# Kernel tuning notes

Hardware: AMD Instinct MI355X
Metric: run time of the kernel (lower is better)

## Reference

```python
import jax, jax.numpy as jnp
import numpy as np

LEAKY = 0.1  # leaky_hmm_coefficient (pychain default)


def _fb_objf(x_exp, tfrom, tto, tpdf, tprob, init_p, final_p):
    """Leaky-HMM forward recursion for one sequence.
    x_exp: [T, P] exp'd nnet outputs; transitions are edge lists of length E.
    Returns scalar log-prob of the sequence under the graph.
    """
    S = init_p.shape[0]

    def step(carry, obs):
        alpha, logz = carry  # alpha: [S] normalized occupation probs
        # per-edge contribution: alpha[src] * trans_prob * obs[pdf]
        contrib = alpha[tfrom] * tprob * obs[tpdf]          # [E]
        new_alpha = jnp.zeros(S, alpha.dtype).at[tto].add(contrib)
        tot = new_alpha.sum()
        # leaky-HMM: redistribute a fraction of total mass via initial probs
        new_alpha = new_alpha + LEAKY * tot * init_p
        scale = new_alpha.sum()
        return (new_alpha / scale, logz + jnp.log(scale)), None

    (alpha_T, logz), _ = jax.lax.scan(step, (init_p, jnp.zeros((), x_exp.dtype)), x_exp)
    return logz + jnp.log(jnp.sum(alpha_T * final_p))


def setup_inputs() -> dict:
    key = jax.random.key(0)
    ks = jax.random.split(key, 12)
    B, T, P = 32, 500, 3000
    S_den, E_den = 2000, 40000
    S_num, E_num = 100, 400

    x = jax.random.normal(ks[0], (B, T, P), jnp.float32)

    # denominator graph (shared across batch); every state gets incoming arcs
    den_to = (jnp.arange(E_den, dtype=jnp.int32) % S_den)
    den_from = jax.random.randint(ks[1], (E_den,), 0, S_den, jnp.int32)
    den_pdf = jax.random.randint(ks[2], (E_den,), 0, P, jnp.int32)
    den_prob = jax.random.uniform(ks[3], (E_den,), jnp.float32, 0.1, 1.0)
    den_init = jax.random.uniform(ks[4], (S_den,), jnp.float32, 0.1, 1.0)
    den_init = den_init / den_init.sum()
    den_final = jax.random.uniform(ks[5], (S_den,), jnp.float32, 0.1, 1.0)

    # numerator graphs (one per utterance), batched edge lists
    num_to = jnp.tile(jnp.arange(E_num, dtype=jnp.int32) % S_num, (B, 1))
    num_from = jax.random.randint(ks[6], (B, E_num), 0, S_num, jnp.int32)
    num_pdf = jax.random.randint(ks[7], (B, E_num), 0, P, jnp.int32)
    num_prob = jax.random.uniform(ks[8], (B, E_num), jnp.float32, 0.1, 1.0)
    num_init = jax.random.uniform(ks[9], (B, S_num), jnp.float32, 0.1, 1.0)
    num_init = num_init / num_init.sum(axis=1, keepdims=True)
    num_final = jax.random.uniform(ks[10], (B, S_num), jnp.float32, 0.1, 1.0)

    return {
        "x": x,
        "den_from": den_from, "den_to": den_to, "den_pdf": den_pdf,
        "den_prob": den_prob, "den_init": den_init, "den_final": den_final,
        "num_from": num_from, "num_to": num_to, "num_pdf": num_pdf,
        "num_prob": num_prob, "num_init": num_init, "num_final": num_final,
    }


def reference(x, den_from, den_to, den_pdf, den_prob, den_init, den_final,
              num_from, num_to, num_pdf, num_prob, num_init, num_final):
    B, T, _ = x.shape
    exp_x = jnp.exp(jnp.clip(x, -30.0, 30.0))  # [B, T, P]

    # denominator: shared graph across batch
    den_objf = jax.vmap(_fb_objf, in_axes=(0, None, None, None, None, None, None))(
        exp_x, den_from, den_to, den_pdf, den_prob, den_init, den_final).sum()
    # numerator: per-utterance graph
    num_objf = jax.vmap(_fb_objf, in_axes=(0, 0, 0, 0, 0, 0, 0))(
        exp_x, num_from, num_to, num_pdf, num_prob, num_init, num_final).sum()

    objf = -(num_objf - den_objf)
    return objf / (B * T)  # avg=True
```

## Files before the change

### kernel.cpp

```cpp
#include <hip/hip_runtime.h>


#define LEAKY 0.1f
#define AGENT __HIP_MEMORY_SCOPE_AGENT

constexpr int B = 32, T = 500, P = 3000;
constexpr int S_DEN = 2000;
constexpr int S_NUM = 100, E_NUM = 400;
constexpr int NTH = 1024;
constexpr int NWAVE = NTH / 64;
constexpr int G_DEN = 5;
constexpr int SB = S_DEN / G_DEN;
constexpr int KE = 20;
constexpr int EPT = KE / 2;
constexpr int OBS_T0 = 800;
constexpr int OBS_N = NTH - OBS_T0;
constexpr int OBS_IT = (P + OBS_N - 1) / OBS_N;
constexpr int KE_NUM = 4;
constexpr int NDEN_BLK = B * G_DEN;


__device__ __forceinline__ float clampexp(float x) {
  return __expf(fminf(fmaxf(x, -30.f), 30.f));
}
__device__ __forceinline__ void st_f32(float* p, float v) {
  __hip_atomic_store(p, v, __ATOMIC_RELAXED, AGENT);
}
__device__ __forceinline__ unsigned long long ld_u64(const float* p) {
  return __hip_atomic_load((const unsigned long long*)p, __ATOMIC_RELAXED,
                           AGENT);
}

__device__ __forceinline__ float reduce_1024(float v, float* wpart) {
#pragma unroll
  for (int off = 32; off; off >>= 1) v += __shfl_xor(v, off, 64);
  if ((threadIdx.x & 63) == 0) wpart[threadIdx.x >> 6] = v;
  __syncthreads();
  float s = 0.f;
#pragma unroll
  for (int w = 0; w < NWAVE; ++w) s += wpart[w];
  return s;
}

__device__ void run_den(const float* __restrict__ xb,
                        const int* __restrict__ ef_g,
                        const int* __restrict__ ep_g,
                        const float* __restrict__ epr_g,
                        const float* __restrict__ einit,
                        const float* __restrict__ efinal, int b, int g,
                        float* __restrict__ outs, float* __restrict__ parts_b,
                        float* obsA, float* obsB, float* cur, float* ini_s,
                        float* tmp, float* wpart) {
  const int tid = threadIdx.x;
  const bool gat = tid < 2 * SB;
  const bool own = tid < SB;
  const bool cons = tid < S_DEN / 2;
  const int jloc = own ? tid : (gat ? tid - SB : 0);
  const int khalf = (tid >= SB && gat) ? 1 : 0;
  const int j = g * SB + jloc;

  float lsum = 0.f;
  if (tid < S_DEN / 2) {
    const float2 iv = ((const float2*)einit)[tid];
    ((float2*)ini_s)[tid] = iv;
    ((float2*)cur)[tid] = iv;
    lsum = iv.x + iv.y;
  }
  __syncthreads();
  const float leakfac = 1.f + LEAKY * reduce_1024(lsum, wpart);

  int efep[EPT];
  float epr[EPT], w[EPT];
  if (gat) {
#pragma unroll
    for (int k = 0; k < EPT; ++k) {
      const int e = j + (khalf * EPT + k) * S_DEN;
      efep[k] = ef_g[e] | (ep_g[e] << 16);
      epr[k] = epr_g[e];
    }
    const int off = (3 * (tid & 63)) & 31;
#pragma unroll
    for (int i = 0; i < EPT - 1; ++i) {
#pragma unroll
      for (int k = 0; k < EPT - 1 - i; ++k) {
        const int ka = ((efep[k] & 31) - off) & 31;
        const int kb = ((efep[k + 1] & 31) - off) & 31;
        if (kb < ka) {
          const int te = efep[k]; efep[k] = efep[k + 1]; efep[k + 1] = te;
          const float tp = epr[k]; epr[k] = epr[k + 1]; epr[k + 1] = tp;
        }
      }
    }
  }

  obsA[tid] = clampexp(xb[tid]);
  obsA[tid + 1024] = clampexp(xb[tid + 1024]);
  if (tid + 2048 < P) obsA[tid + 2048] = clampexp(xb[tid + 2048]);
  float xr[OBS_IT];
  if (tid >= OBS_T0) {
    const float* r = xb + P;
#pragma unroll
    for (int i = 0; i < OBS_IT; ++i) {
      const int p = tid - OBS_T0 + OBS_N * i;
      xr[i] = (p < P) ? r[p] : 0.f;
    }
  }
  __syncthreads();
  if (gat) {
#pragma unroll
    for (int k = 0; k < EPT; ++k) w[k] = epr[k] * obsA[efep[k] >> 16];
  }

  float logz = 0.f;
  for (int t = 0; t < T; ++t) {
    const int par = t & 1;
    float* obs_n = par ? obsA : obsB;
    float a = 0.f;
    if (gat) {
#pragma unroll
      for (int k = 0; k < EPT; ++k) a += cur[efep[k] & 0xffff] * w[k];
      if (!own) tmp[jloc] = a;
    } else if (tid >= OBS_T0) {
      float nxr[OBS_IT];
      const int tn = (t + 2 < T) ? t + 2 : T - 1;
      const float* r = xb + (size_t)tn * P;
#pragma unroll
      for (int i = 0; i < OBS_IT; ++i) {
        const int p = tid - OBS_T0 + OBS_N * i;
        nxr[i] = (p < P) ? r[p] : 0.f;
      }
      if (t + 1 < T) {
#pragma unroll
        for (int i = 0; i < OBS_IT; ++i) {
          const int p = tid - OBS_T0 + OBS_N * i;
          if (p < P) obs_n[p] = clampexp(xr[i]);
        }
      }
#pragma unroll
      for (int i = 0; i < OBS_IT; ++i) xr[i] = nxr[i];
    }
    __syncthreads();
    const unsigned tag = ((unsigned)t >> 1) & 1u;
    if (own) {
      const float aa = a + tmp[tid];
      st_f32(parts_b + par * 2048 + j, tag ? -aa : aa);
    }
    const float* myp = parts_b + par * 2048 + 2 * tid;
    unsigned long long u = 0;
    if (cons) u = ld_u64(myp);
    if (gat && t + 1 < T) {
#pragma unroll
      for (int k = 0; k < EPT; ++k) w[k] = epr[k] * obs_n[efep[k] >> 16];
    }
    if (cons) {
      while ((((unsigned)(u >> 31) & 1u) != tag) ||
             (((unsigned)(u >> 63) & 1u) != tag)) {
        __builtin_amdgcn_s_sleep(1);
        u = ld_u64(myp);
      }
    }
    union { unsigned long long q; float2 f; } cc;
    cc.q = u;
    const float2 v2 = make_float2(fabsf(cc.f.x), fabsf(cc.f.y));
    const float tot = reduce_1024(v2.x + v2.y, wpart);
    const float scale = tot * leakfac;
    const float inv = 1.f / scale, lt = LEAKY * tot;
    if (cons) {
      const float2 i2 = ((const float2*)ini_s)[tid];
      ((float2*)cur)[tid] = make_float2(fmaf(lt, i2.x, v2.x) * inv,
                                        fmaf(lt, i2.y, v2.y) * inv);
    }
    logz += __logf(scale);
    __syncthreads();
  }

  float fv = 0.f;
  if (tid < S_DEN / 2) {
    const float2 f2 = ((const float2*)efinal)[tid];
    const float2 c2 = ((float2*)cur)[tid];
    fv = c2.x * f2.x + c2.y * f2.y;
  }
  const float fin = reduce_1024(fv, wpart);
  if (tid == 0 && g == 0) outs[b] = logz + __logf(fin);
}

__device__ void run_num(const float* __restrict__ xb, const int* __restrict__ ef,
                        const int* __restrict__ ep, const float* __restrict__ epr,
                        const float* __restrict__ einit,
                        const float* __restrict__ efinal,
                        float* __restrict__ out_slot, float* __restrict__ obs,
                        float* __restrict__ cur, float* __restrict__ wpart) {
  const int tid = threadIdx.x;
  const bool act = tid < S_NUM / 2;
  const int j = 2 * tid;
  float2 ini = make_float2(0.f, 0.f), fin2 = make_float2(0.f, 0.f);
  if (act) {
    ini = ((const float2*)einit)[tid];
    fin2 = ((const float2*)efinal)[tid];
  }
  __syncthreads();
  const float leakfac =
      1.f + LEAKY * reduce_1024(act ? ini.x + ini.y : 0.f, wpart);

  int2 f2[KE_NUM], p2[KE_NUM];
  float2 pr2[KE_NUM];
  if (act) {
#pragma unroll
    for (int k = 0; k < KE_NUM; ++k) {
      f2[k] = ((const int2*)(ef + k * S_NUM))[tid];
      p2[k] = ((const int2*)(ep + k * S_NUM))[tid];
      pr2[k] = ((const float2*)(epr + k * S_NUM))[tid];
    }
  }
  obs[tid] = clampexp(xb[tid]);
  obs[tid + 1024] = clampexp(xb[tid + 1024]);
  if (tid + 2048 < P) obs[tid + 2048] = clampexp(xb[tid + 2048]);
  float xr0, xr1, xr2;
  {
    const float* r = xb + P;
    xr0 = r[tid];
    xr1 = r[tid + 1024];
    xr2 = (tid + 2048 < P) ? r[tid + 2048] : 0.f;
  }
  if (act) {
    cur[j] = ini.x;
    cur[j + 1] = ini.y;
  }
  __syncthreads();

  float logz = 0.f;
  for (int t = 0; t < T; ++t) {
    float nx0 = xr0, nx1 = xr1, nx2 = xr2;
    if (t + 2 < T) {
      const float* r = xb + (size_t)(t + 2) * P;
      nx0 = r[tid];
      nx1 = r[tid + 1024];
      nx2 = (tid + 2048 < P) ? r[tid + 2048] : 0.f;
    }
    float a0 = 0.f, a1 = 0.f;
    if (act) {
#pragma unroll
      for (int k = 0; k < KE_NUM; ++k) {
        a0 += cur[f2[k].x] * pr2[k].x * obs[p2[k].x];
        a1 += cur[f2[k].y] * pr2[k].y * obs[p2[k].y];
      }
    }
    float v = a0 + a1;
#pragma unroll
    for (int off = 32; off; off >>= 1) v += __shfl_xor(v, off, 64);
    if ((tid & 63) == 0) wpart[tid >> 6] = v;
    __syncthreads();
    float tot = 0.f;
#pragma unroll
    for (int w = 0; w < NWAVE; ++w) tot += wpart[w];
    if (t + 1 < T) {
      obs[tid] = clampexp(xr0);
      obs[tid + 1024] = clampexp(xr1);
      if (tid + 2048 < P) obs[tid + 2048] = clampexp(xr2);
    }
    xr0 = nx0;
    xr1 = nx1;
    xr2 = nx2;
    const float scale = tot * leakfac;
    const float inv = 1.f / scale, lt = LEAKY * tot;
    if (act) {
      cur[j] = fmaf(lt, ini.x, a0) * inv;
      cur[j + 1] = fmaf(lt, ini.y, a1) * inv;
    }
    logz += __logf(scale);
    __syncthreads();
  }
  __syncthreads();
  const float fin = reduce_1024(
      act ? (cur[j] * fin2.x + cur[j + 1] * fin2.y) : 0.f, wpart);
  if (tid == 0) *out_slot = logz + __logf(fin);
}

__global__ __launch_bounds__(NTH) void fb_kernel(
    const float* __restrict__ x, const int* __restrict__ den_from,
    const int* __restrict__ den_pdf, const float* __restrict__ den_prob,
    const float* __restrict__ den_init, const float* __restrict__ den_final,
    const int* __restrict__ num_from, const int* __restrict__ num_pdf,
    const float* __restrict__ num_prob, const float* __restrict__ num_init,
    const float* __restrict__ num_final, float* __restrict__ ws) {
  __shared__ float obsA[P];
  __shared__ float obsB[P];
  __shared__ float cur[S_DEN];
  __shared__ float ini_s[S_DEN];
  __shared__ float tmp[SB];
  __shared__ float wpart[NWAVE];
  float* outs = ws;
  float* parts = ws + 4096;
  const int blk = blockIdx.x;
  if (blk < NDEN_BLK) {
    const int b = blk / G_DEN, g = blk % G_DEN;
    run_den(x + (size_t)b * T * P, den_from, den_pdf, den_prob, den_init,
            den_final, b, g, outs, parts + (size_t)b * 4096, obsA, obsB, cur,
            ini_s, tmp, wpart);
  } else {
    const int b = blk - NDEN_BLK;
    run_num(x + (size_t)b * T * P, num_from + b * E_NUM, num_pdf + b * E_NUM,
            num_prob + b * E_NUM, num_init + b * S_NUM, num_final + b * S_NUM,
            outs + B + b, obsA, cur, wpart);
  }
}

__global__ void init_parts(float* p) {
  st_f32(&p[blockIdx.x * NTH + threadIdx.x], -1.f);
}

__global__ void finish_kernel(const float* __restrict__ ws,
                              float* __restrict__ out) {
  const int tid = threadIdx.x;
  float v = ws[tid];
  v = (tid < B) ? v : -v;
#pragma unroll
  for (int off = 32; off; off >>= 1) v += __shfl_xor(v, off, 64);
  if (tid == 0) out[0] = v / (float)(B * T);
}

extern "C" void kernel_launch(void* const* d_in, const int* in_sizes, int n_in,
                              void* d_out, int out_size, void* d_ws,
                              size_t ws_size, hipStream_t stream) {
  const float* x = (const float*)d_in[0];
  const int* den_from = (const int*)d_in[1];
  const int* den_pdf = (const int*)d_in[3];
  const float* den_prob = (const float*)d_in[4];
  const float* den_init = (const float*)d_in[5];
  const float* den_final = (const float*)d_in[6];
  const int* num_from = (const int*)d_in[7];
  const int* num_pdf = (const int*)d_in[9];
  const float* num_prob = (const float*)d_in[10];
  const float* num_init = (const float*)d_in[11];
  const float* num_final = (const float*)d_in[12];
  float* ws = (float*)d_ws;
  float* out = (float*)d_out;

  init_parts<<<(B * 4096) / NTH, NTH, 0, stream>>>(ws + 4096);
  fb_kernel<<<NDEN_BLK + B, NTH, 0, stream>>>(
      x, den_from, den_pdf, den_prob, den_init, den_final, num_from, num_pdf,
      num_prob, num_init, num_final, ws);
  finish_kernel<<<1, 64, 0, stream>>>(ws, out);
}
```

Measured before the change: 1.618 ms.

## Defer leaky normalization into gather step and cut per-step barriers in den recursion

Restructures the denominator time loop so the two edge halves of each state sit on adjacent lanes and combine through a shuffle, replacing the shared tmp array and its extra barrier. The per-step normalization (total, leak term, scale) is deferred to the next step: the raw unnormalized alpha is stored, and the next gather applies inv*(a + lt*ini-weighted term), using a precomputed per-edge ini*prob coefficient. The block reduction is split so partial sums are written in one step and consumed after the next barrier, removing one __syncthreads per timestep. The cost is extra per-edge FMAs for the ini-weighted term and a changed parity/tag scheme for the cross-block exchange buffer, which needs init_parts to change to match.

```diff
diff --git a/kernel.cpp b/kernel.cpp
--- a/kernel.cpp
+++ b/kernel.cpp
@@ -50,35 +50,34 @@
                         const float* __restrict__ efinal, int b, int g,
                         float* __restrict__ outs, float* __restrict__ parts_b,
                         float* obsA, float* obsB, float* cur, float* ini_s,
-                        float* tmp, float* wpart) {
+                        float* wpart) {
   const int tid = threadIdx.x;
+  const int lane = tid & 63;
   const bool gat = tid < 2 * SB;
-  const bool own = tid < SB;
   const bool cons = tid < S_DEN / 2;
-  const int jloc = own ? tid : (gat ? tid - SB : 0);
-  const int khalf = (tid >= SB && gat) ? 1 : 0;
+  const int jloc = (tid >> 6) * 32 + (lane >> 1);
+  const int half = lane & 1;
   const int j = g * SB + jloc;
 
   float lsum = 0.f;
-  if (tid < S_DEN / 2) {
+  if (cons) {
     const float2 iv = ((const float2*)einit)[tid];
     ((float2*)ini_s)[tid] = iv;
-    ((float2*)cur)[tid] = iv;
     lsum = iv.x + iv.y;
   }
   __syncthreads();
   const float leakfac = 1.f + LEAKY * reduce_1024(lsum, wpart);
 
   int efep[EPT];
-  float epr[EPT], w[EPT];
+  float epr[EPT], w[EPT], c[EPT];
   if (gat) {
 #pragma unroll
     for (int k = 0; k < EPT; ++k) {
-      const int e = j + (khalf * EPT + k) * S_DEN;
+      const int e = j + (half * EPT + k) * S_DEN;
       efep[k] = ef_g[e] | (ep_g[e] << 16);
       epr[k] = epr_g[e];
     }
-    const int off = (3 * (tid & 63)) & 31;
+    const int off = (3 * lane) & 31;
 #pragma unroll
     for (int i = 0; i < EPT - 1; ++i) {
 #pragma unroll
@@ -91,6 +90,8 @@
         }
       }
     }
+#pragma unroll
+    for (int k = 0; k < EPT; ++k) c[k] = ini_s[efep[k] & 0xffff] * epr[k];
   }
 
   obsA[tid] = clampexp(xb[tid]);
@@ -106,20 +107,43 @@
     }
   }
   __syncthreads();
+  float iniw = 0.f;
   if (gat) {
 #pragma unroll
-    for (int k = 0; k < EPT; ++k) w[k] = epr[k] * obsA[efep[k] >> 16];
+    for (int k = 0; k < EPT; ++k) {
+      const float o = obsA[efep[k] >> 16];
+      w[k] = epr[k] * o;
+      iniw += c[k] * o;
+    }
   }
 
   float logz = 0.f;
+  float lt = 0.f, inv = 0.f;
   for (int t = 0; t < T; ++t) {
-    const int par = t & 1;
-    float* obs_n = par ? obsA : obsB;
-    float a = 0.f;
+    float* obs_n = (t & 1) ? obsA : obsB;
+    float a_raw = 0.f;
+    if (t) {
+      if (gat) {
+#pragma unroll
+        for (int k = 0; k < EPT; ++k) a_raw += cur[efep[k] & 0xffff] * w[k];
+      }
+      float s = 0.f;
+#pragma unroll
+      for (int wv = 0; wv < NWAVE; ++wv) s += wpart[wv];
+      const float scale = s * leakfac;
+      lt = LEAKY * s;
+      inv = 1.f / scale;
+      logz += __logf(scale);
+    }
+    const int parn = (t + 1) & 1;
+    const unsigned tagn = ((unsigned)(t + 1) >> 1) & 1u;
     if (gat) {
-#pragma unroll
-      for (int k = 0; k < EPT; ++k) a += cur[efep[k] & 0xffff] * w[k];
-      if (!own) tmp[jloc] = a;
+      const float ar = a_raw + __shfl_xor(a_raw, 1, 64);
+      const float iw = iniw + __shfl_xor(iniw, 1, 64);
+      if (!half) {
+        const float aa = t ? inv * fmaf(lt, iw, ar) : iw;
+        st_f32(parts_b + parn * 2048 + j, tagn ? -aa : aa);
+      }
     } else if (tid >= OBS_T0) {
       float nxr[OBS_IT];
       const int tn = (t + 2 < T) ? t + 2 : T - 1;
@@ -140,21 +164,21 @@
       for (int i = 0; i < OBS_IT; ++i) xr[i] = nxr[i];
     }
     __syncthreads();
-    const unsigned tag = ((unsigned)t >> 1) & 1u;
-    if (own) {
-      const float aa = a + tmp[tid];
-      st_f32(parts_b + par * 2048 + j, tag ? -aa : aa);
-    }
-    const float* myp = parts_b + par * 2048 + 2 * tid;
+    const float* myp = parts_b + parn * 2048 + 2 * tid;
     unsigned long long u = 0;
     if (cons) u = ld_u64(myp);
     if (gat && t + 1 < T) {
-#pragma unroll
-      for (int k = 0; k < EPT; ++k) w[k] = epr[k] * obs_n[efep[k] >> 16];
+      iniw = 0.f;
+#pragma unroll
+      for (int k = 0; k < EPT; ++k) {
+        const float o = obs_n[efep[k] >> 16];
+        w[k] = epr[k] * o;
+        iniw += c[k] * o;
+      }
     }
     if (cons) {
-      while ((((unsigned)(u >> 31) & 1u) != tag) ||
-             (((unsigned)(u >> 63) & 1u) != tag)) {
+      while ((((unsigned)(u >> 31) & 1u) != tagn) ||
+             (((unsigned)(u >> 63) & 1u) != tagn)) {
         __builtin_amdgcn_s_sleep(1);
         u = ld_u64(myp);
       }
@@ -162,24 +186,29 @@
     union { unsigned long long q; float2 f; } cc;
     cc.q = u;
     const float2 v2 = make_float2(fabsf(cc.f.x), fabsf(cc.f.y));
-    const float tot = reduce_1024(v2.x + v2.y, wpart);
-    const float scale = tot * leakfac;
-    const float inv = 1.f / scale, lt = LEAKY * tot;
-    if (cons) {
-      const float2 i2 = ((const float2*)ini_s)[tid];
-      ((float2*)cur)[tid] = make_float2(fmaf(lt, i2.x, v2.x) * inv,
-                                        fmaf(lt, i2.y, v2.y) * inv);
-    }
-    logz += __logf(scale);
+    float pv = cons ? (v2.x + v2.y) : 0.f;
+#pragma unroll
+    for (int off2 = 32; off2; off2 >>= 1) pv += __shfl_xor(pv, off2, 64);
+    if (lane == 0) wpart[tid >> 6] = pv;
+    if (cons) ((float2*)cur)[tid] = v2;
     __syncthreads();
   }
 
+  float s = 0.f;
+#pragma unroll
+  for (int wv = 0; wv < NWAVE; ++wv) s += wpart[wv];
+  const float scaleT = s * leakfac;
+  logz += __logf(scaleT);
+  const float ltT = LEAKY * s, invT = 1.f / scaleT;
   float fv = 0.f;
-  if (tid < S_DEN / 2) {
+  if (cons) {
     const float2 f2 = ((const float2*)efinal)[tid];
-    const float2 c2 = ((float2*)cur)[tid];
-    fv = c2.x * f2.x + c2.y * f2.y;
-  }
+    const float2 i2 = ((const float2*)ini_s)[tid];
+    const float2 c2 = ((const float2*)cur)[tid];
+    fv = (fmaf(ltT, i2.x, c2.x) * invT) * f2.x +
+         (fmaf(ltT, i2.y, c2.y) * invT) * f2.y;
+  }
+  __syncthreads();
   const float fin = reduce_1024(fv, wpart);
   if (tid == 0 && g == 0) outs[b] = logz + __logf(fin);
 }
@@ -287,7 +316,6 @@
   __shared__ float obsB[P];
   __shared__ float cur[S_DEN];
   __shared__ float ini_s[S_DEN];
-  __shared__ float tmp[SB];
   __shared__ float wpart[NWAVE];
   float* outs = ws;
   float* parts = ws + 4096;
@@ -296,7 +324,7 @@
     const int b = blk / G_DEN, g = blk % G_DEN;
     run_den(x + (size_t)b * T * P, den_from, den_pdf, den_prob, den_init,
             den_final, b, g, outs, parts + (size_t)b * 4096, obsA, obsB, cur,
-            ini_s, tmp, wpart);
+            ini_s, wpart);
   } else {
     const int b = blk - NDEN_BLK;
     run_num(x + (size_t)b * T * P, num_from + b * E_NUM, num_pdf + b * E_NUM,
@@ -306,7 +334,8 @@
 }
 
 __global__ void init_parts(float* p) {
-  st_f32(&p[blockIdx.x * NTH + threadIdx.x], -1.f);
+  const int i = blockIdx.x * NTH + threadIdx.x;
+  st_f32(&p[i], ((i >> 11) & 1) ? -1.f : 1.f);
 }
 
 __global__ void finish_kernel(const float* __restrict__ ws,
```

Result: faster. 1.335 ms (-17.5%).
